# Performance work log

Measured on AMD Instinct MI355X. Metric: run time of the kernel, lower is better.

Reference implementation:

```python
import jax, jax.numpy as jnp
import numpy as np

B, T, C, H, R = 4, 2048, 1024, 16, 64
D = C // H  # head_dim = 64
ALPHA = 0.7  # init_alpha; alpha_proj is None so c_proj also uses 0.7


def _harmonic_linear(x, U, V):
    # W = U @ diag(s) @ V with harmonic decay s_k = (k+1)^{-alpha}; y = x @ W^T
    s = (jnp.arange(R, dtype=x.dtype) + 1.0) ** (-ALPHA)
    return ((x @ V.T) * s) @ U.T


def setup_inputs() -> dict:
    key = jax.random.key(0)
    ks = jax.random.split(key, 9)
    p = lambda k, shape: 0.02 * jax.random.normal(k, shape, dtype=jnp.float32)
    return {
        "x": jax.random.normal(ks[0], (B, T, C), dtype=jnp.float32),
        "q_U": p(ks[1], (C, R)), "q_V": p(ks[2], (R, C)),
        "k_U": p(ks[3], (C, R)), "k_V": p(ks[4], (R, C)),
        "v_U": p(ks[5], (C, R)), "v_V": p(ks[6], (R, C)),
        "c_U": p(ks[7], (C, R)), "c_V": p(ks[8], (R, C)),
    }


def reference(x, q_U, q_V, k_U, k_V, v_U, v_V, c_U, c_V):
    # projections -> [B, H, T, D]
    def split_heads(t):
        return t.reshape(B, T, H, D).transpose(0, 2, 1, 3)

    q = split_heads(_harmonic_linear(x, q_U, q_V))
    k = split_heads(_harmonic_linear(x, k_U, k_V))
    v = split_heads(_harmonic_linear(x, v_U, v_V))

    scale = 1.0 / np.sqrt(D).astype(np.float32)
    att = jnp.einsum("bhqd,bhkd->bhqk", q, k) * scale  # [B,H,T,T]
    causal = jnp.tril(jnp.ones((T, T), dtype=bool))
    att = jnp.where(causal[None, None], att, jnp.finfo(att.dtype).min)
    att = jax.nn.softmax(att, axis=-1)  # dropout p=0.0 -> identity

    y = jnp.einsum("bhqk,bhkd->bhqd", att, v)  # [B,H,T,D]
    y = y.transpose(0, 2, 1, 3).reshape(B, T, C)
    return _harmonic_linear(y, c_U, c_V)
```

## Files before the change

kernel.cpp:

```cpp
#include <hip/hip_runtime.h>
#include <hip/hip_bf16.h>
#include <math.h>


#define NB 4
#define NT 2048
#define NC 1024
#define NH 16
#define NR 64
#define ND 64
#define NM (NB * NT)

typedef __attribute__((ext_vector_type(8))) short short8;
typedef __attribute__((ext_vector_type(4))) short short4v;
typedef __attribute__((ext_vector_type(4))) float f32x4;
typedef __attribute__((ext_vector_type(4))) float float4v;
typedef __attribute__((ext_vector_type(4))) int int4v;

__device__ __forceinline__ short f2bf(float f) {
    union { __hip_bfloat16 h; short s; } u;
    u.h = __float2bfloat16(f);
    return u.s;
}
__device__ __forceinline__ float bf2f(short s) {
    union { short s; __hip_bfloat16 h; } u;
    u.s = s;
    return __bfloat162float(u.h);
}
__device__ __forceinline__ f32x4 MFMA(short8 a, short8 b, f32x4 c) {
    return __builtin_amdgcn_mfma_f32_16x16x32_bf16(a, b, c, 0, 0, 0);
}
__device__ __forceinline__ float exp2_(float x) {
#if __has_builtin(__builtin_amdgcn_exp2f)
    return __builtin_amdgcn_exp2f(x);
#else
    return exp2f(x);
#endif
}

typedef const __attribute__((address_space(1))) unsigned int* gas_ptr;
typedef __attribute__((address_space(3))) unsigned int* las_ptr;
__device__ __forceinline__ void gll16(const void* g, void* l) {
    __builtin_amdgcn_global_load_lds((gas_ptr)g, (las_ptr)l, 16, 0, 0);
}

__global__ __launch_bounds__(256) void k_prep(const float* __restrict__ qV, const float* __restrict__ kV,
                                              const float* __restrict__ vV, const float* __restrict__ cV,
                                              const float* __restrict__ qU, const float* __restrict__ kU,
                                              const float* __restrict__ vU, const float* __restrict__ cU,
                                              short* __restrict__ Whi, short* __restrict__ Wlo) {
    const int idx = blockIdx.x * 256 + threadIdx.x;
    const int mat = idx >> 13;
    const int f = idx & 8191;
    const int l = f & 63;
    const int rest = f >> 6;
    const float* src;
    switch (mat) {
        case 0: src = qV; break;
        case 1: src = kV; break;
        case 2: src = vV; break;
        case 3: src = cV; break;
        case 4: src = qU; break;
        case 5: src = kU; break;
        case 6: src = vU; break;
        default: src = cU; break;
    }
    int row, col, stride;
    if (mat < 4) {
        const int s = rest & 31, nt = rest >> 5;
        row = nt * 16 + (l & 15);
        col = s * 32 + (l >> 4) * 8;
        stride = NC;
    } else {
        const int ks = rest & 1, tn = rest >> 1;
        row = tn * 16 + (l & 15);
        col = ks * 32 + (l >> 4) * 8;
        stride = NR;
    }
    float sc = 1.0f;
    if (mat < 4) sc = powf((float)(row + 1), -0.7f);
    if (mat == 4) sc = 0.125f * 1.44269504088896f;
    const float* p = src + (size_t)row * stride + col;
    const float4v a = *(const float4v*)p;
    const float4v b = *(const float4v*)(p + 4);
    float v[8] = {a[0], a[1], a[2], a[3], b[0], b[1], b[2], b[3]};
    short* oh = Whi + (size_t)mat * 65536 + (size_t)f * 8;
    short* ol = Wlo + (size_t)mat * 65536 + (size_t)f * 8;
    short4v h0, h1, l0, l1;
#pragma unroll
    for (int j = 0; j < 8; j++) {
        const float fv = v[j] * sc;
        const short h = f2bf(fv);
        const short lo = f2bf(fv - bf2f(h));
        if (j < 4) { h0[j] = h; l0[j] = lo; } else { h1[j - 4] = h; l1[j - 4] = lo; }
    }
    *(short4v*)oh = h0;
    *(short4v*)(oh + 4) = h1;
    *(short4v*)ol = l0;
    *(short4v*)(ol + 4) = l1;
}

__global__ __launch_bounds__(512, 2) void k_qkv(const float* __restrict__ X,
                                                const short* __restrict__ Whi, const short* __restrict__ Wlo,
                                                short* __restrict__ qb, short* __restrict__ kb,
                                                short* __restrict__ vtb) {
    __shared__ __align__(16) char Xl[2][16384];
    __shared__ __align__(16) short Thi[32 * 200];
    __shared__ __align__(16) short Tlov[32 * 72];
    const int tid = threadIdx.x;
    const int w = tid >> 6, l = tid & 63;
    const int lr = l & 15, lk = l >> 4;
    const int g = w & 3, mg = w >> 2;
    const int mb = blockIdx.x * 32;

    auto stageX = [&](int buf, int win) {
#pragma unroll
        for (int q = 0; q < 2; q++) {
            const int r = q * 16 + w * 2 + (l >> 5);
            const int c = l & 31;
            const int sc16 = c ^ (r & 15);
            const float* gp = X + (size_t)(mb + r) * NC + win * 128 + sc16 * 4;
            gll16(gp, (char*)Xl[buf] + q * 8192 + w * 1024);
        }
    };

    const short* Wqk_f = (g < 2) ? Whi : (Whi + 65536);
    const int tA = ((g & 1) * 2) * 32;
    const int tB = tA + 32;
    const int tV = g * 32;
    const short* vfh = Whi + 2 * 65536;
    const short* vfl = Wlo + 2 * 65536;

    f32x4 a0 = 0.0f, a1 = 0.0f, av = 0.0f;
    const int xrow = (mg * 16 + lr) * 512;
    stageX(0, 0);
    for (int win = 0; win < 8; ++win) {
        const int buf = win & 1;
        __syncthreads();
        if (win < 7) stageX(buf ^ 1, win + 1);
        const char* XB = Xl[buf];
#pragma unroll
        for (int kk = 0; kk < 4; ++kk) {
            const int cb = kk * 8 + lk * 2;
            const float4v xa = *(const float4v*)(XB + xrow + ((cb ^ lr) << 4));
            const float4v xb = *(const float4v*)(XB + xrow + (((cb + 1) ^ lr) << 4));
            float xv[8] = {xa[0], xa[1], xa[2], xa[3], xb[0], xb[1], xb[2], xb[3]};
            short8 xh, xl8;
#pragma unroll
            for (int j = 0; j < 8; j++) {
                const short h = f2bf(xv[j]);
                xh[j] = h;
                xl8[j] = f2bf(xv[j] - bf2f(h));
            }
            const int s = win * 4 + kk;
            const short8 wa = *(const short8*)(Wqk_f + (size_t)((tA + s) * 64 + l) * 8);
            const short8 wb = *(const short8*)(Wqk_f + (size_t)((tB + s) * 64 + l) * 8);
            const short8 wvh = *(const short8*)(vfh + (size_t)((tV + s) * 64 + l) * 8);
            const short8 wvl = *(const short8*)(vfl + (size_t)((tV + s) * 64 + l) * 8);
            a0 = MFMA(xh, wa, a0);
            a1 = MFMA(xh, wb, a1);
            av = MFMA(xh, wvh, av);
            av = MFMA(xh, wvl, av);
            av = MFMA(xl8, wvh, av);
        }
    }
    {
        const int p = g >> 1;
        const int colA = p * 64 + (g & 1) * 32 + lr;
        const int colB = colA + 16;
        const int colV = 128 + g * 16 + lr;
#pragma unroll
        for (int i = 0; i < 4; i++) {
            const int row = mg * 16 + lk * 4 + i;
            Thi[row * 200 + colA] = f2bf(a0[i]);
            Thi[row * 200 + colB] = f2bf(a1[i]);
            const short hv = f2bf(av[i]);
            Thi[row * 200 + colV] = hv;
            Tlov[row * 72 + g * 16 + lr] = f2bf(av[i] - bf2f(hv));
        }
    }
    __syncthreads();
    const short* qUf = Whi + 4 * 65536;
    const short* kUf = Whi + 5 * 65536;
    const short* vUfh = Whi + 6 * 65536;
    const short* vUfl = Wlo + 6 * 65536;
    short8 tf[2][3][2];
    short8 tfl[2][2];
#pragma unroll
    for (int m2 = 0; m2 < 2; m2++) {
        const int trow = m2 * 16 + lr;
#pragma unroll
        for (int ks = 0; ks < 2; ks++) {
#pragma unroll
            for (int p = 0; p < 3; p++)
                tf[m2][p][ks] = *(const short8*)(Thi + trow * 200 + p * 64 + ks * 32 + lk * 8);
            tfl[m2][ks] = *(const short8*)(Tlov + trow * 72 + ks * 32 + lk * 8);
        }
    }
    const int bb = mb >> 11, mt = mb & (NT - 1);
#pragma unroll 2
    for (int nt = 0; nt < 8; nt++) {
        const int tn = w * 8 + nt;
        short8 uq[2], uk[2], uvh[2], uvl[2];
#pragma unroll
        for (int ks = 0; ks < 2; ks++) {
            const size_t off = (size_t)((tn * 2 + ks) * 64 + l) * 8;
            uq[ks] = *(const short8*)(qUf + off);
            uk[ks] = *(const short8*)(kUf + off);
            uvh[ks] = *(const short8*)(vUfh + off);
            uvl[ks] = *(const short8*)(vUfl + off);
        }
#pragma unroll
        for (int m2 = 0; m2 < 2; m2++) {
            f32x4 aq = 0.0f, ak = 0.0f, avv = 0.0f;
#pragma unroll
            for (int ks = 0; ks < 2; ks++) {
                aq = MFMA(uq[ks], tf[m2][0][ks], aq);
                ak = MFMA(uk[ks], tf[m2][1][ks], ak);
                avv = MFMA(tf[m2][2][ks], uvh[ks], avv);
                avv = MFMA(tf[m2][2][ks], uvl[ks], avv);
                avv = MFMA(tfl[m2][ks], uvh[ks], avv);
            }
            const int tt = mt + m2 * 16 + lr;
            const int nq = tn * 16 + lk * 4;
            const int hhq = nq >> 6, ddq = nq & 63;
            short4v pq, pk;
#pragma unroll
            for (int i = 0; i < 4; i++) { pq[i] = f2bf(aq[i]); pk[i] = f2bf(ak[i]); }
            *(short4v*)(qb + ((size_t)(bb * NH + hhq) * NT + tt) * ND + ddq) = pq;
            *(short4v*)(kb + ((size_t)(bb * NH + hhq) * NT + tt) * ND + ddq) = pk;
            const int n = tn * 16 + lr;
            const int hhv = n >> 6, ddv = n & 63;
            const int tv = mt + m2 * 16 + lk * 4;
            short4v pv;
#pragma unroll
            for (int i = 0; i < 4; i++) pv[i] = f2bf(avv[i]);
            *(short4v*)(vtb + ((size_t)(bb * NH + hhv) * ND + ddv) * NT + tv) = pv;
        }
    }
}

__global__ __launch_bounds__(512, 2) void k_cout(const short* __restrict__ Yb,
                                                 const short* __restrict__ Whi, const short* __restrict__ Wlo,
                                                 float* __restrict__ Out) {
    __shared__ __align__(16) char Yl[2][16384];
    __shared__ __align__(16) short tyhi[32 * 72];
    __shared__ __align__(16) short tylo[32 * 72];
    const int tid = threadIdx.x;
    const int w = tid >> 6, l = tid & 63;
    const int lr = l & 15, lk = l >> 4;
    const int g = w & 3, mg = w >> 2;
    const int mb = blockIdx.x * 32;
    const short* cVfh = Whi + 3 * 65536;
    const short* cVfl = Wlo + 3 * 65536;
    const short* cUfh = Whi + 7 * 65536;
    const short* cUfl = Wlo + 7 * 65536;

    auto stageY = [&](int buf, int win) {
#pragma unroll
        for (int q = 0; q < 2; q++) {
            const int r = q * 16 + w * 2 + (l >> 5);
            const int c = l & 31;
            const int sc16 = c ^ (r & 15);
            const short* gp = Yb + (size_t)(mb + r) * NC + win * 256 + sc16 * 8;
            gll16(gp, (char*)Yl[buf] + q * 8192 + w * 1024);
        }
    };

    const int tV = g * 32;
    f32x4 acc = 0.0f;
    const int xrow = (mg * 16 + lr) * 512;
    stageY(0, 0);
    for (int win = 0; win < 4; ++win) {
        const int buf = win & 1;
        __syncthreads();
        if (win < 3) stageY(buf ^ 1, win + 1);
        const char* YB = Yl[buf];
#pragma unroll
        for (int kk = 0; kk < 8; ++kk) {
            const short8 ah = *(const short8*)(YB + xrow + ((((kk * 4 + lk)) ^ lr) << 4));
            const int s = win * 8 + kk;
            const short8 wh = *(const short8*)(cVfh + (size_t)((tV + s) * 64 + l) * 8);
            const short8 wl = *(const short8*)(cVfl + (size_t)((tV + s) * 64 + l) * 8);
            acc = MFMA(ah, wh, acc);
            acc = MFMA(ah, wl, acc);
        }
    }
#pragma unroll
    for (int i = 0; i < 4; i++) {
        const int row = mg * 16 + lk * 4 + i;
        const short h = f2bf(acc[i]);
        tyhi[row * 72 + g * 16 + lr] = h;
        tylo[row * 72 + g * 16 + lr] = f2bf(acc[i] - bf2f(h));
    }
    __syncthreads();
    short8 th[2][2], tl[2][2];
#pragma unroll
    for (int m2 = 0; m2 < 2; m2++) {
        const int trow = m2 * 16 + lr;
#pragma unroll
        for (int ks = 0; ks < 2; ks++) {
            th[m2][ks] = *(const short8*)(tyhi + trow * 72 + ks * 32 + lk * 8);
            tl[m2][ks] = *(const short8*)(tylo + trow * 72 + ks * 32 + lk * 8);
        }
    }
#pragma unroll 2
    for (int nt = 0; nt < 8; nt++) {
        const int tn = w * 8 + nt;
        short8 uh[2], ul[2];
#pragma unroll
        for (int ks = 0; ks < 2; ks++) {
            const size_t off = (size_t)((tn * 2 + ks) * 64 + l) * 8;
            uh[ks] = *(const short8*)(cUfh + off);
            ul[ks] = *(const short8*)(cUfl + off);
        }
#pragma unroll
        for (int m2 = 0; m2 < 2; m2++) {
            f32x4 a = 0.0f;
#pragma unroll
            for (int ks = 0; ks < 2; ks++) {
                a = MFMA(uh[ks], th[m2][ks], a);
                a = MFMA(ul[ks], th[m2][ks], a);
                a = MFMA(uh[ks], tl[m2][ks], a);
            }
            const int mm = mb + m2 * 16 + lr;
            const int n = tn * 16 + lk * 4;
            *(float4v*)(Out + (size_t)mm * NC + n) = *(float4v*)&a;
        }
    }
}

__device__ __forceinline__ short8 lds_frag(const short* base, int row, int cb) {
    return *(const short8*)((const char*)base + (((row << 7) + cb) ^ ((row & 7) << 4)));
}

__global__ __launch_bounds__(256, 4) void k_attn(const short* __restrict__ Qm,
                                                 const short* __restrict__ Km,
                                                 const short* __restrict__ Vt,
                                                 short* __restrict__ Y) {
    __shared__ __align__(16) short Kl[2][64 * 64];
    __shared__ __align__(16) short Vl[2][64 * 64];
    __shared__ __align__(16) short Pl[4 * 1024];
    const int tid = threadIdx.x;
    const int w = tid >> 6, l = tid & 63;
    const int lr = l & 15, lk = l >> 4;
    const int lin = blockIdx.y * 16 + blockIdx.x;
    const int nl = (lin & 7) * 128 + (lin >> 3);
    const int j = nl & 15;
    const int bh = nl >> 4;
    const int ntile = 32 - j;
    const int qA = 64 * j + w * 16;
    const int qB = (NT - 64 * (j + 1)) + w * 16;
    const int qrel = w * 16 + lr;

    const short* Kb = Km + (size_t)bh * NT * ND;
    const short* Vb = Vt + (size_t)bh * ND * NT;

    short8 qfA[2], qfB[2];
#pragma unroll
    for (int ks = 0; ks < 2; ks++) {
        qfA[ks] = *(const short8*)(Qm + ((size_t)bh * NT + qA + lr) * ND + ks * 32 + lk * 8);
        qfB[ks] = *(const short8*)(Qm + ((size_t)bh * NT + qB + lr) * ND + ks * 32 + lk * 8);
    }

    const int grow8 = w * 8 + (l >> 3);
    const int gcolb = (((l & 7) ^ ((l >> 3) & 7)) << 4);
    auto stage = [&](int buf, int kv0) {
        const char* kp = (const char*)Kb + (((size_t)(kv0 + grow8)) << 7) + gcolb;
        const char* vp = (const char*)Vb + (size_t)grow8 * (NT * 2) + kv0 * 2 + gcolb;
        char* kl = (char*)Kl[buf] + w * 1024;
        char* vl = (char*)Vl[buf] + w * 1024;
        gll16(kp, kl);
        gll16(kp + (32 << 7), kl + 4096);
        gll16(vp, vl);
        gll16(vp + (size_t)32 * NT * 2, vl + 4096);
    };

    f32x4 lsA = 0.0f, lsB = 0.0f;
    f32x4 oA[4], oB[4];
#pragma unroll
    for (int dt = 0; dt < 4; dt++) { oA[dt] = 0.0f; oB[dt] = 0.0f; }

    char* plb = (char*)Pl + w * 2048;

    auto compute = [&](const short8* qf, f32x4& ls, f32x4* o,
                       const short* KlB, const short* VlB, bool diag) {
        f32x4 sa[4];
#pragma unroll
        for (int nt = 0; nt < 4; nt++) sa[nt] = -16.0f;
        __builtin_amdgcn_s_setprio(1);
#pragma unroll
        for (int ks = 0; ks < 2; ks++) {
#pragma unroll
            for (int nt = 0; nt < 4; nt++) {
                const short8 kf = lds_frag(KlB, nt * 16 + lr, ks * 64 + lk * 16);
                sa[nt] = MFMA(kf, qf[ks], sa[nt]);
            }
        }
        __builtin_amdgcn_s_setprio(0);
        if (diag) {
#pragma unroll
            for (int nt = 0; nt < 4; nt++) {
                const int kvb = nt * 16 + lk * 4;
#pragma unroll
                for (int i = 0; i < 4; i++)
                    if (kvb + i > qrel) sa[nt][i] = -1e30f;
            }
        }
        f32x4 sv[4];
#pragma unroll
        for (int nt = 0; nt < 4; nt++) {
#pragma unroll
            for (int i = 0; i < 4; i++) sv[nt][i] = exp2_(sa[nt][i]);
            ls += sv[nt];
        }
#pragma unroll
        for (int nt = 0; nt < 4; nt++) {
            short4v pk;
#pragma unroll
            for (int i = 0; i < 4; i++) pk[i] = f2bf(sv[nt][i]);
            *(short4v*)(plb + (((lr << 7) + ((nt * 16 + lk * 4) << 1)) ^ ((lr & 7) << 4))) = pk;
        }
        const short8 pb0 = *(const short8*)(plb + (((lr << 7) + ((lk * 8) << 1)) ^ ((lr & 7) << 4)));
        const short8 pb1 = *(const short8*)(plb + (((lr << 7) + ((32 + lk * 8) << 1)) ^ ((lr & 7) << 4)));
        __builtin_amdgcn_s_setprio(1);
#pragma unroll
        for (int ks = 0; ks < 2; ks++) {
            const short8 pb = ks ? pb1 : pb0;
#pragma unroll
            for (int dt = 0; dt < 4; dt++) {
                const short8 vf = lds_frag(VlB, dt * 16 + lr, ks * 64 + lk * 16);
                o[dt] = MFMA(vf, pb, o[dt]);
            }
        }
        __builtin_amdgcn_s_setprio(0);
    };

    stage(0, 0);
    for (int it = 0; it < ntile; ++it) {
        const int buf = it & 1;
        __syncthreads();
        if (it + 1 < ntile) stage(buf ^ 1, (it + 1) * 64);
        const short* KlB = Kl[buf];
        const short* VlB = Vl[buf];
        if (it <= j) compute(qfA, lsA, oA, KlB, VlB, it == j);
        compute(qfB, lsB, oB, KlB, VlB, it == ntile - 1);
    }

    float lA = (lsA[0] + lsA[1]) + (lsA[2] + lsA[3]);
    float lB = (lsB[0] + lsB[1]) + (lsB[2] + lsB[3]);
    lA += __shfl_xor(lA, 16);
    lA += __shfl_xor(lA, 32);
    lB += __shfl_xor(lB, 16);
    lB += __shfl_xor(lB, 32);

    const int b = bh >> 4, h = bh & 15;
    const float invA = 1.0f / lA, invB = 1.0f / lB;
    short* ypA = Y + ((size_t)b * NT + (qA + lr)) * NC + h * ND;
    short* ypB = Y + ((size_t)b * NT + (qB + lr)) * NC + h * ND;
#pragma unroll
    for (int dt = 0; dt < 4; dt++) {
        short4v ya, yb2;
#pragma unroll
        for (int i = 0; i < 4; i++) {
            ya[i] = f2bf(oA[dt][i] * invA);
            yb2[i] = f2bf(oB[dt][i] * invB);
        }
        *(short4v*)(ypA + dt * 16 + lk * 4) = ya;
        *(short4v*)(ypB + dt * 16 + lk * 4) = yb2;
    }
}

extern "C" void kernel_launch(void* const* d_in, const int* in_sizes, int n_in,
                              void* d_out, int out_size, void* d_ws, size_t ws_size,
                              hipStream_t stream) {
    const float* x = (const float*)d_in[0];
    const float* qU = (const float*)d_in[1];
    const float* qV = (const float*)d_in[2];
    const float* kU = (const float*)d_in[3];
    const float* kV = (const float*)d_in[4];
    const float* vU = (const float*)d_in[5];
    const float* vV = (const float*)d_in[6];
    const float* cU = (const float*)d_in[7];
    const float* cV = (const float*)d_in[8];
    float* out = (float*)d_out;

    char* ws = (char*)d_ws;
    size_t off = 0;
    auto take = [&](size_t bytes) {
        char* p = ws + off;
        off += (bytes + 255) & ~(size_t)255;
        return p;
    };
    short* Whi = (short*)take(8 * 65536 * 2);
    short* Wlo = (short*)take(8 * 65536 * 2);
    short* qb = (short*)take((size_t)NM * NC * 2);
    short* kb = (short*)take((size_t)NM * NC * 2);
    short* vtb = (short*)take((size_t)NM * NC * 2);
    short* yb = (short*)take((size_t)NM * NC * 2);

    k_prep<<<256, 256, 0, stream>>>(qV, kV, vV, cV, qU, kU, vU, cU, Whi, Wlo);
    k_qkv<<<256, 512, 0, stream>>>(x, Whi, Wlo, qb, kb, vtb);
    k_attn<<<dim3(16, NB * NH), 256, 0, stream>>>(qb, kb, vtb, yb);
    k_cout<<<256, 512, 0, stream>>>(yb, Whi, Wlo, out);
}
```

Baseline: 118.6 us.

## Process 128-row query tiles per attention block with two fragments per wave

Each attention workgroup now covers 128 query rows per paired causal tile instead of 64, with each wave holding two 16-row query fragments that share every K and V LDS fragment read. This halves the grid and the number of K/V tile loads per query, cutting global and LDS traffic per unit of work. In exchange, register pressure and the P scratch buffer double, the launch bound drops to 2 blocks per CU, and causal masking becomes per-wave diagonals, which adds some imbalance inside each block.

```diff
diff --git a/kernel.cpp b/kernel.cpp
--- a/kernel.cpp
+++ b/kernel.cpp
@@ -147,10 +147,10 @@
             float xv[8] = {xa[0], xa[1], xa[2], xa[3], xb[0], xb[1], xb[2], xb[3]};
             short8 xh, xl8;
 #pragma unroll
-            for (int j = 0; j < 8; j++) {
-                const short h = f2bf(xv[j]);
-                xh[j] = h;
-                xl8[j] = f2bf(xv[j] - bf2f(h));
+            for (int jj = 0; jj < 8; jj++) {
+                const short h = f2bf(xv[jj]);
+                xh[jj] = h;
+                xl8[jj] = f2bf(xv[jj] - bf2f(h));
             }
             const int s = win * 4 + kk;
             const short8 wa = *(const short8*)(Wqk_f + (size_t)((tA + s) * 64 + l) * 8);
@@ -204,11 +204,11 @@
         short8 uq[2], uk[2], uvh[2], uvl[2];
 #pragma unroll
         for (int ks = 0; ks < 2; ks++) {
-            const size_t off = (size_t)((tn * 2 + ks) * 64 + l) * 8;
-            uq[ks] = *(const short8*)(qUf + off);
-            uk[ks] = *(const short8*)(kUf + off);
-            uvh[ks] = *(const short8*)(vUfh + off);
-            uvl[ks] = *(const short8*)(vUfl + off);
+            const size_t off2 = (size_t)((tn * 2 + ks) * 64 + l) * 8;
+            uq[ks] = *(const short8*)(qUf + off2);
+            uk[ks] = *(const short8*)(kUf + off2);
+            uvh[ks] = *(const short8*)(vUfh + off2);
+            uvl[ks] = *(const short8*)(vUfl + off2);
         }
 #pragma unroll
         for (int m2 = 0; m2 < 2; m2++) {
@@ -310,9 +310,9 @@
         short8 uh[2], ul[2];
 #pragma unroll
         for (int ks = 0; ks < 2; ks++) {
-            const size_t off = (size_t)((tn * 2 + ks) * 64 + l) * 8;
-            uh[ks] = *(const short8*)(cUfh + off);
-            ul[ks] = *(const short8*)(cUfl + off);
+            const size_t off2 = (size_t)((tn * 2 + ks) * 64 + l) * 8;
+            uh[ks] = *(const short8*)(cUfh + off2);
+            ul[ks] = *(const short8*)(cUfl + off2);
         }
 #pragma unroll
         for (int m2 = 0; m2 < 2; m2++) {
@@ -334,33 +334,37 @@
     return *(const short8*)((const char*)base + (((row << 7) + cb) ^ ((row & 7) << 4)));
 }
 
-__global__ __launch_bounds__(256, 4) void k_attn(const short* __restrict__ Qm,
+__global__ __launch_bounds__(256, 2) void k_attn(const short* __restrict__ Qm,
                                                  const short* __restrict__ Km,
                                                  const short* __restrict__ Vt,
                                                  short* __restrict__ Y) {
     __shared__ __align__(16) short Kl[2][64 * 64];
     __shared__ __align__(16) short Vl[2][64 * 64];
-    __shared__ __align__(16) short Pl[4 * 1024];
+    __shared__ __align__(16) short Pl[8 * 1024];
     const int tid = threadIdx.x;
     const int w = tid >> 6, l = tid & 63;
     const int lr = l & 15, lk = l >> 4;
-    const int lin = blockIdx.y * 16 + blockIdx.x;
-    const int nl = (lin & 7) * 128 + (lin >> 3);
-    const int j = nl & 15;
-    const int bh = nl >> 4;
-    const int ntile = 32 - j;
-    const int qA = 64 * j + w * 16;
-    const int qB = (NT - 64 * (j + 1)) + w * 16;
-    const int qrel = w * 16 + lr;
+    const int lin = blockIdx.y * 8 + blockIdx.x;
+    const int nl = (lin & 7) * 64 + (lin >> 3);
+    const int j = nl & 7;
+    const int bh = nl >> 3;
+    const int ntile = 32 - 2 * j;
+    const int qA0 = 128 * j + w * 32;
+    const int qB0 = (1920 - 128 * j) + w * 32;
+    const int diagA = 2 * j + (w >> 1);
+    const int diagB = 30 - 2 * j + (w >> 1);
 
     const short* Kb = Km + (size_t)bh * NT * ND;
     const short* Vb = Vt + (size_t)bh * ND * NT;
 
-    short8 qfA[2], qfB[2];
-#pragma unroll
-    for (int ks = 0; ks < 2; ks++) {
-        qfA[ks] = *(const short8*)(Qm + ((size_t)bh * NT + qA + lr) * ND + ks * 32 + lk * 8);
-        qfB[ks] = *(const short8*)(Qm + ((size_t)bh * NT + qB + lr) * ND + ks * 32 + lk * 8);
+    short8 qfA[2][2], qfB[2][2];
+#pragma unroll
+    for (int f = 0; f < 2; f++) {
+#pragma unroll
+        for (int ks = 0; ks < 2; ks++) {
+            qfA[f][ks] = *(const short8*)(Qm + ((size_t)bh * NT + qA0 + f * 16 + lr) * ND + ks * 32 + lk * 8);
+            qfB[f][ks] = *(const short8*)(Qm + ((size_t)bh * NT + qB0 + f * 16 + lr) * ND + ks * 32 + lk * 8);
+        }
     }
 
     const int grow8 = w * 8 + (l >> 3);
@@ -376,61 +380,77 @@
         gll16(vp + (size_t)32 * NT * 2, vl + 4096);
     };
 
-    f32x4 lsA = 0.0f, lsB = 0.0f;
-    f32x4 oA[4], oB[4];
-#pragma unroll
-    for (int dt = 0; dt < 4; dt++) { oA[dt] = 0.0f; oB[dt] = 0.0f; }
-
-    char* plb = (char*)Pl + w * 2048;
-
-    auto compute = [&](const short8* qf, f32x4& ls, f32x4* o,
-                       const short* KlB, const short* VlB, bool diag) {
-        f32x4 sa[4];
-#pragma unroll
-        for (int nt = 0; nt < 4; nt++) sa[nt] = -16.0f;
+    f32x4 lsA[2], lsB[2];
+    f32x4 oA[2][4], oB[2][4];
+#pragma unroll
+    for (int f = 0; f < 2; f++) {
+        lsA[f] = 0.0f;
+        lsB[f] = 0.0f;
+#pragma unroll
+        for (int dt = 0; dt < 4; dt++) { oA[f][dt] = 0.0f; oB[f][dt] = 0.0f; }
+    }
+
+    auto computeG = [&](const short8 (&qf)[2][2], f32x4 (&ls)[2], f32x4 (&o)[2][4],
+                        const short* KlB, const short* VlB, bool diag) {
+        f32x4 sa[2][4];
+#pragma unroll
+        for (int f = 0; f < 2; f++)
+#pragma unroll
+            for (int nt = 0; nt < 4; nt++) sa[f][nt] = -16.0f;
         __builtin_amdgcn_s_setprio(1);
 #pragma unroll
         for (int ks = 0; ks < 2; ks++) {
 #pragma unroll
             for (int nt = 0; nt < 4; nt++) {
                 const short8 kf = lds_frag(KlB, nt * 16 + lr, ks * 64 + lk * 16);
-                sa[nt] = MFMA(kf, qf[ks], sa[nt]);
+                sa[0][nt] = MFMA(kf, qf[0][ks], sa[0][nt]);
+                sa[1][nt] = MFMA(kf, qf[1][ks], sa[1][nt]);
             }
         }
         __builtin_amdgcn_s_setprio(0);
         if (diag) {
 #pragma unroll
+            for (int f = 0; f < 2; f++) {
+                const int qrel = (w & 1) * 32 + f * 16 + lr;
+#pragma unroll
+                for (int nt = 0; nt < 4; nt++) {
+                    const int kvb = nt * 16 + lk * 4;
+#pragma unroll
+                    for (int i = 0; i < 4; i++)
+                        if (kvb + i > qrel) sa[f][nt][i] = -1e30f;
+                }
+            }
+        }
+#pragma unroll
+        for (int f = 0; f < 2; f++) {
+            char* plbf = (char*)Pl + w * 4096 + f * 2048;
+#pragma unroll
             for (int nt = 0; nt < 4; nt++) {
-                const int kvb = nt * 16 + lk * 4;
-#pragma unroll
-                for (int i = 0; i < 4; i++)
-                    if (kvb + i > qrel) sa[nt][i] = -1e30f;
-            }
-        }
-        f32x4 sv[4];
-#pragma unroll
-        for (int nt = 0; nt < 4; nt++) {
-#pragma unroll
-            for (int i = 0; i < 4; i++) sv[nt][i] = exp2_(sa[nt][i]);
-            ls += sv[nt];
-        }
-#pragma unroll
-        for (int nt = 0; nt < 4; nt++) {
-            short4v pk;
-#pragma unroll
-            for (int i = 0; i < 4; i++) pk[i] = f2bf(sv[nt][i]);
-            *(short4v*)(plb + (((lr << 7) + ((nt * 16 + lk * 4) << 1)) ^ ((lr & 7) << 4))) = pk;
-        }
-        const short8 pb0 = *(const short8*)(plb + (((lr << 7) + ((lk * 8) << 1)) ^ ((lr & 7) << 4)));
-        const short8 pb1 = *(const short8*)(plb + (((lr << 7) + ((32 + lk * 8) << 1)) ^ ((lr & 7) << 4)));
+                f32x4 sv;
+#pragma unroll
+                for (int i = 0; i < 4; i++) sv[i] = exp2_(sa[f][nt][i]);
+                ls[f] += sv;
+                short4v pk;
+#pragma unroll
+                for (int i = 0; i < 4; i++) pk[i] = f2bf(sv[i]);
+                *(short4v*)(plbf + (((lr << 7) + ((nt * 16 + lk * 4) << 1)) ^ ((lr & 7) << 4))) = pk;
+            }
+        }
+        short8 pb[2][2];
+#pragma unroll
+        for (int f = 0; f < 2; f++) {
+            const char* plbf = (const char*)Pl + w * 4096 + f * 2048;
+            pb[f][0] = *(const short8*)(plbf + (((lr << 7) + ((lk * 8) << 1)) ^ ((lr & 7) << 4)));
+            pb[f][1] = *(const short8*)(plbf + (((lr << 7) + ((32 + lk * 8) << 1)) ^ ((lr & 7) << 4)));
+        }
         __builtin_amdgcn_s_setprio(1);
 #pragma unroll
         for (int ks = 0; ks < 2; ks++) {
-            const short8 pb = ks ? pb1 : pb0;
 #pragma unroll
             for (int dt = 0; dt < 4; dt++) {
                 const short8 vf = lds_frag(VlB, dt * 16 + lr, ks * 64 + lk * 16);
-                o[dt] = MFMA(vf, pb, o[dt]);
+                o[0][dt] = MFMA(vf, pb[0][ks], o[0][dt]);
+                o[1][dt] = MFMA(vf, pb[1][ks], o[1][dt]);
             }
         }
         __builtin_amdgcn_s_setprio(0);
@@ -443,31 +463,33 @@
         if (it + 1 < ntile) stage(buf ^ 1, (it + 1) * 64);
         const short* KlB = Kl[buf];
         const short* VlB = Vl[buf];
-        if (it <= j) compute(qfA, lsA, oA, KlB, VlB, it == j);
-        compute(qfB, lsB, oB, KlB, VlB, it == ntile - 1);
-    }
-
-    float lA = (lsA[0] + lsA[1]) + (lsA[2] + lsA[3]);
-    float lB = (lsB[0] + lsB[1]) + (lsB[2] + lsB[3]);
-    lA += __shfl_xor(lA, 16);
-    lA += __shfl_xor(lA, 32);
-    lB += __shfl_xor(lB, 16);
-    lB += __shfl_xor(lB, 32);
+        if (it <= diagA) computeG(qfA, lsA, oA, KlB, VlB, it == diagA);
+        if (it <= diagB) computeG(qfB, lsB, oB, KlB, VlB, it == diagB);
+    }
 
     const int b = bh >> 4, h = bh & 15;
-    const float invA = 1.0f / lA, invB = 1.0f / lB;
-    short* ypA = Y + ((size_t)b * NT + (qA + lr)) * NC + h * ND;
-    short* ypB = Y + ((size_t)b * NT + (qB + lr)) * NC + h * ND;
-#pragma unroll
-    for (int dt = 0; dt < 4; dt++) {
-        short4v ya, yb2;
-#pragma unroll
-        for (int i = 0; i < 4; i++) {
-            ya[i] = f2bf(oA[dt][i] * invA);
-            yb2[i] = f2bf(oB[dt][i] * invB);
-        }
-        *(short4v*)(ypA + dt * 16 + lk * 4) = ya;
-        *(short4v*)(ypB + dt * 16 + lk * 4) = yb2;
+#pragma unroll
+    for (int f = 0; f < 2; f++) {
+        float lA = (lsA[f][0] + lsA[f][1]) + (lsA[f][2] + lsA[f][3]);
+        float lB = (lsB[f][0] + lsB[f][1]) + (lsB[f][2] + lsB[f][3]);
+        lA += __shfl_xor(lA, 16);
+        lA += __shfl_xor(lA, 32);
+        lB += __shfl_xor(lB, 16);
+        lB += __shfl_xor(lB, 32);
+        const float invA = 1.0f / lA, invB = 1.0f / lB;
+        short* ypA = Y + ((size_t)b * NT + (qA0 + f * 16 + lr)) * NC + h * ND;
+        short* ypB = Y + ((size_t)b * NT + (qB0 + f * 16 + lr)) * NC + h * ND;
+#pragma unroll
+        for (int dt = 0; dt < 4; dt++) {
+            short4v ya, yb2;
+#pragma unroll
+            for (int i = 0; i < 4; i++) {
+                ya[i] = f2bf(oA[f][dt][i] * invA);
+                yb2[i] = f2bf(oB[f][dt][i] * invB);
+            }
+            *(short4v*)(ypA + dt * 16 + lk * 4) = ya;
+            *(short4v*)(ypB + dt * 16 + lk * 4) = yb2;
+        }
     }
 }
 
@@ -501,6 +523,6 @@
 
     k_prep<<<256, 256, 0, stream>>>(qV, kV, vV, cV, qU, kU, vU, cU, Whi, Wlo);
     k_qkv<<<256, 512, 0, stream>>>(x, Whi, Wlo, qb, kb, vtb);
-    k_attn<<<dim3(16, NB * NH), 256, 0, stream>>>(qb, kb, vtb, yb);
+    k_attn<<<dim3(8, NB * NH), 256, 0, stream>>>(qb, kb, vtb, yb);
     k_cout<<<256, 512, 0, stream>>>(yb, Whi, Wlo, out);
 }
```

Measured after the change: 117.8 us, median of 3. Within noise of the previous version (-0.6%).
